# Kernel tuning notes

Hardware: AMD Instinct MI355X
Metric: run time of the kernel (lower is better)

The kernel has to match this reference:

```python
import jax, jax.numpy as jnp
import numpy as np

N_SAMPLES = 2048
BURN_IN = 128
STEP_SIZE = 0.1
D = 512   # walker dimension
H = 1024  # wavefunction MLP hidden width


def setup_inputs() -> dict:
    key = jax.random.key(0)
    k0, k1, k2 = jax.random.split(key, 3)
    x0 = jax.random.normal(k0, (1, D), dtype=jnp.float32)
    W1 = jax.random.normal(k1, (D, H), dtype=jnp.float32) / np.float32(np.sqrt(D))
    b1 = jnp.zeros((H,), dtype=jnp.float32)
    W2 = jax.random.normal(k2, (H, 1), dtype=jnp.float32) / np.float32(np.sqrt(H))
    b2 = jnp.zeros((1,), dtype=jnp.float32)
    return {"x0": x0, "W1": W1, "b1": b1, "W2": W2, "b2": b2}


def _model(x, W1, b1, W2, b2):
    # wavefunction MLP: [1, D] -> [1, 1]
    return jnp.tanh(x @ W1 + b1) @ W2 + b2


def reference(x0, W1, b1, W2, b2):
    def psi2(x):
        # model(x).pow(2)[0] -> shape [1]
        return (_model(x, W1, b1, W2, b2) ** 2)[0]

    def mh_step(x, k):
        k_noise, k_unif = jax.random.split(k)
        x_new = x + jax.random.normal(k_noise, x.shape, dtype=x.dtype) * STEP_SIZE
        p_new = psi2(x_new)
        p_old = psi2(x)
        ratio = jnp.minimum(p_new / (p_old + 1e-12), 1.0)          # clamp(max=1.0)
        u = jax.random.uniform(k_unif, ratio.shape, dtype=x.dtype)
        accept = (u < ratio).astype(x.dtype)[:, None]               # [1, 1]
        x = accept * x_new + (1.0 - accept) * x
        return x, x[0]  # carry chain state, record sample row [D]

    keys = jax.random.split(jax.random.key(1), N_SAMPLES + BURN_IN)
    _, traj = jax.lax.scan(mh_step, x0, keys)   # traj: [N+BURN_IN, D]
    return traj[BURN_IN:]                        # [N_SAMPLES, D]
```

## Files before the change

kernel.cpp:

```cpp
#include <hip/hip_runtime.h>
#include <stdint.h>
#include <math.h>


#define T_TOTAL 2176
#define NITER   1088
#define NROWS   2177
#define NBURN   128
#define DDIM    512
#define HDIM    1024
#define DONE_FLAG 0x13572468u

__device__ __forceinline__ uint2 tf2x32(uint32_t k0, uint32_t k1,
                                        uint32_t x0, uint32_t x1) {
  uint32_t ks2 = k0 ^ k1 ^ 0x1BD11BDAu;
  x0 += k0; x1 += k1;
#define TF_R(r) { x0 += x1; x1 = (x1 << (r)) | (x1 >> (32 - (r))); x1 ^= x0; }
  TF_R(13) TF_R(15) TF_R(26) TF_R(6)
  x0 += k1;  x1 += ks2 + 1u;
  TF_R(17) TF_R(29) TF_R(16) TF_R(24)
  x0 += ks2; x1 += k0 + 2u;
  TF_R(13) TF_R(15) TF_R(26) TF_R(6)
  x0 += k0;  x1 += k1 + 3u;
  TF_R(17) TF_R(29) TF_R(16) TF_R(24)
  x0 += k1;  x1 += ks2 + 4u;
  TF_R(13) TF_R(15) TF_R(26) TF_R(6)
  x0 += ks2; x1 += k0 + 5u;
#undef TF_R
  return make_uint2(x0, x1);
}

__device__ __forceinline__ float erfinv_xla(float x) {
  float w = -log1pf(-x * x);
  float p;
  if (w < 5.0f) {
    w = w - 2.5f;
    p = 2.81022636e-08f;
    p = fmaf(p, w, 3.43273939e-07f);
    p = fmaf(p, w, -3.5233877e-06f);
    p = fmaf(p, w, -4.39150654e-06f);
    p = fmaf(p, w, 0.00021858087f);
    p = fmaf(p, w, -0.00125372503f);
    p = fmaf(p, w, -0.00417768164f);
    p = fmaf(p, w, 0.246640727f);
    p = fmaf(p, w, 1.50140941f);
  } else {
    w = sqrtf(w) - 3.0f;
    p = -0.000200214257f;
    p = fmaf(p, w, 0.000100950558f);
    p = fmaf(p, w, 0.00134934322f);
    p = fmaf(p, w, -0.00367342844f);
    p = fmaf(p, w, 0.00573950773f);
    p = fmaf(p, w, -0.0076224613f);
    p = fmaf(p, w, 0.00943887047f);
    p = fmaf(p, w, 1.00167406f);
    p = fmaf(p, w, 2.83297682f);
  }
  return p * x;
}

__device__ __forceinline__ float normal_from_bits(uint32_t bits) {
  const float lo = -0.99999994f;
  float u01 = __uint_as_float(0x3f800000u | (bits >> 9)) - 1.0f;
  float v = u01 * 2.0f + lo;
  v = fmaxf(lo, v);
  return 1.41421356237309515f * erfinv_xla(v);
}

#if __has_builtin(__builtin_amdgcn_exp2f)
#define EXP2F __builtin_amdgcn_exp2f
#else
#define EXP2F exp2f
#endif
#define RCPF __builtin_amdgcn_rcpf
#define TANH_C 2.88539008177792681472f

__device__ __forceinline__ float tanh_fast(float x) {
  float a = x * TANH_C;
  float e = EXP2F(a);
  float r = RCPF(e + 1.0f);
  return fmaf(-2.0f, r, 1.0f);
}

__global__ void __launch_bounds__(256) rng_kernel(const float* __restrict__ x0,
                                                  float* __restrict__ A,
                                                  double* __restrict__ A64,
                                                  float* __restrict__ U) {
  const uint32_t t = blockIdx.x;
  const int tid = threadIdx.x;
  uint2 kt = tf2x32(0u, 1u, 0u, t);
  uint2 kn = tf2x32(kt.x, kt.y, 0u, 0u);
  uint2 e0 = tf2x32(kn.x, kn.y, 0u, (uint32_t)tid);
  uint2 e1 = tf2x32(kn.x, kn.y, 0u, (uint32_t)(tid + 256));
  float n0 = normal_from_bits(e0.x ^ e0.y) * 0.1f;
  float n1 = normal_from_bits(e1.x ^ e1.y) * 0.1f;
  float* Arow = A + (size_t)(t + 1) * DDIM;
  Arow[tid]       = n0;
  Arow[tid + 256] = n1;
  if (A64) {
    double* Arow64 = A64 + (size_t)(t + 1) * DDIM;
    Arow64[tid]       = (double)n0;
    Arow64[tid + 256] = (double)n1;
  }
  if (tid == 0) {
    uint2 ku = tf2x32(kt.x, kt.y, 0u, 1u);
    uint2 eu = tf2x32(ku.x, ku.y, 0u, 0u);
    U[t] = __uint_as_float(0x3f800000u | ((eu.x ^ eu.y) >> 9)) - 1.0f;
  }
  if (t == 0) {
    float xv0 = x0[tid], xv1 = x0[tid + 256];
    A[tid]       = xv0;
    A[tid + 256] = xv1;
    if (A64) {
      A64[tid]       = (double)xv0;
      A64[tid + 256] = (double)xv1;
    }
  }
}

__global__ void __launch_bounds__(512) gemm64_kernel(
    const double* __restrict__ A64, const float* __restrict__ W1,
    float* __restrict__ Z, int nrows) {
  const int r0 = blockIdx.x * 4;
  const int t  = threadIdx.x;
  const int c0 = t, c1 = t + 512;
  double acc[4][2];
#pragma unroll
  for (int r = 0; r < 4; ++r) { acc[r][0] = 0.0; acc[r][1] = 0.0; }
  for (int d = 0; d < 512; d += 4) {
    double wA[4], wB[4];
#pragma unroll
    for (int j = 0; j < 4; ++j) {
      wA[j] = (double)W1[(size_t)(d + j) * 1024 + c0];
      wB[j] = (double)W1[(size_t)(d + j) * 1024 + c1];
    }
#pragma unroll
    for (int r = 0; r < 4; ++r) {
      int rr = r0 + r; if (rr >= nrows) rr = nrows - 1;
      const double2 a01 = *(const double2*)(A64 + (size_t)rr * 512 + d);
      const double2 a23 = *(const double2*)(A64 + (size_t)rr * 512 + d + 2);
      acc[r][0] += (a01.x * wA[0] + a01.y * wA[1]) +
                   (a23.x * wA[2] + a23.y * wA[3]);
      acc[r][1] += (a01.x * wB[0] + a01.y * wB[1]) +
                   (a23.x * wB[2] + a23.y * wB[3]);
    }
  }
  const int rmax = (nrows - r0 < 4) ? (nrows - r0) : 4;
  for (int r = 0; r < rmax; ++r) {
    Z[(size_t)(r0 + r) * 1024 + c0] = (float)acc[r][0];
    Z[(size_t)(r0 + r) * 1024 + c1] = (float)acc[r][1];
  }
}

__global__ void __launch_bounds__(512) gemm_kernel(const float* __restrict__ A,
                                                   const float* __restrict__ W1,
                                                   float* __restrict__ Z,
                                                   int nrows) {
  const int r0 = blockIdx.x * 4;
  const int t  = threadIdx.x;
  const int c0 = t, c1 = t + 512;
  double acc[4][2];
#pragma unroll
  for (int r = 0; r < 4; ++r) { acc[r][0] = 0.0; acc[r][1] = 0.0; }
  for (int d = 0; d < 512; d += 4) {
    double wA[4], wB[4];
#pragma unroll
    for (int j = 0; j < 4; ++j) {
      wA[j] = (double)W1[(size_t)(d + j) * 1024 + c0];
      wB[j] = (double)W1[(size_t)(d + j) * 1024 + c1];
    }
#pragma unroll
    for (int r = 0; r < 4; ++r) {
      int rr = r0 + r; if (rr >= nrows) rr = nrows - 1;
      const float4 a4 = *(const float4*)(A + (size_t)rr * 512 + d);
      double a0 = (double)a4.x, a1 = (double)a4.y;
      double a2 = (double)a4.z, a3 = (double)a4.w;
      acc[r][0] += (a0 * wA[0] + a1 * wA[1]) + (a2 * wA[2] + a3 * wA[3]);
      acc[r][1] += (a0 * wB[0] + a1 * wB[1]) + (a2 * wB[2] + a3 * wB[3]);
    }
  }
  const int rmax = (nrows - r0 < 4) ? (nrows - r0) : 4;
  for (int r = 0; r < rmax; ++r) {
    Z[(size_t)(r0 + r) * 1024 + c0] = (float)acc[r][0];
    Z[(size_t)(r0 + r) * 1024 + c1] = (float)acc[r][1];
  }
}

#define DPP_STEP(v, ctrl)                                                    \
  v += __int_as_float(__builtin_amdgcn_update_dpp(                           \
      0, __float_as_int(v), (ctrl), 0xF, 0xF, true))

__device__ __forceinline__ float wave_reduce_to_last(float v) {
  DPP_STEP(v, 0xB1);
  DPP_STEP(v, 0x4E);
  DPP_STEP(v, 0x141);
  DPP_STEP(v, 0x140);
  DPP_STEP(v, 0x142);
  DPP_STEP(v, 0x143);
  return v;
}

__device__ __forceinline__ void wave_reduce3(float& a, float& b, float& c) {
#define R3(ctrl) { DPP_STEP(a, ctrl); DPP_STEP(b, ctrl); DPP_STEP(c, ctrl); }
  R3(0xB1) R3(0x4E) R3(0x141) R3(0x140) R3(0x142) R3(0x143)
#undef R3
}

__device__ __forceinline__ float psidot(double q0, double q1, double q2,
                                        double q3, float4 w2v) {
  float g0 = tanh_fast((float)q0), g1 = tanh_fast((float)q1);
  float g2 = tanh_fast((float)q2), g3 = tanh_fast((float)q3);
  return fmaf(g3, w2v.w, fmaf(g2, w2v.z, fmaf(g1, w2v.y, g0 * w2v.x)));
}

#define BAR() asm volatile("s_waitcnt lgkmcnt(0)\n\ts_barrier" ::: "memory")

#define EVAL3(NXT)                                                           \
  {                                                                          \
    float xA0 = (float)Ya0, xB0 = (float)Yb0, xC0 = (float)Yc0;              \
    float xA1 = (float)Ya1, xB1 = (float)Yb1, xC1 = (float)Yc1;              \
    float xA2 = (float)Ya2, xB2 = (float)Yb2, xC2 = (float)Yc2;              \
    float xA3 = (float)Ya3, xB3 = (float)Yb3, xC3 = (float)Yc3;              \
    float aA0 = xA0 * TANH_C, aB0 = xB0 * TANH_C, aC0 = xC0 * TANH_C;        \
    float aA1 = xA1 * TANH_C, aB1 = xB1 * TANH_C, aC1 = xC1 * TANH_C;        \
    float aA2 = xA2 * TANH_C, aB2 = xB2 * TANH_C, aC2 = xC2 * TANH_C;        \
    float aA3 = xA3 * TANH_C, aB3 = xB3 * TANH_C, aC3 = xC3 * TANH_C;        \
    float eA0 = EXP2F(aA0), eB0 = EXP2F(aB0), eC0 = EXP2F(aC0);              \
    float eA1 = EXP2F(aA1), eB1 = EXP2F(aB1), eC1 = EXP2F(aC1);              \
    float eA2 = EXP2F(aA2), eB2 = EXP2F(aB2), eC2 = EXP2F(aC2);              \
    float eA3 = EXP2F(aA3), eB3 = EXP2F(aB3), eC3 = EXP2F(aC3);              \
    float sA0 = eA0 + 1.0f, sB0 = eB0 + 1.0f, sC0 = eC0 + 1.0f;              \
    float sA1 = eA1 + 1.0f, sB1 = eB1 + 1.0f, sC1 = eC1 + 1.0f;              \
    float sA2 = eA2 + 1.0f, sB2 = eB2 + 1.0f, sC2 = eC2 + 1.0f;              \
    float sA3 = eA3 + 1.0f, sB3 = eB3 + 1.0f, sC3 = eC3 + 1.0f;              \
    float rA0 = RCPF(sA0), rB0 = RCPF(sB0), rC0 = RCPF(sC0);                 \
    float rA1 = RCPF(sA1), rB1 = RCPF(sB1), rC1 = RCPF(sC1);                 \
    float rA2 = RCPF(sA2), rB2 = RCPF(sB2), rC2 = RCPF(sC2);                 \
    float rA3 = RCPF(sA3), rB3 = RCPF(sB3), rC3 = RCPF(sC3);                 \
    float gA0 = fmaf(-2.0f, rA0, 1.0f), gB0 = fmaf(-2.0f, rB0, 1.0f);        \
    float gC0 = fmaf(-2.0f, rC0, 1.0f);                                      \
    float gA1 = fmaf(-2.0f, rA1, 1.0f), gB1 = fmaf(-2.0f, rB1, 1.0f);        \
    float gC1 = fmaf(-2.0f, rC1, 1.0f);                                      \
    float gA2 = fmaf(-2.0f, rA2, 1.0f), gB2 = fmaf(-2.0f, rB2, 1.0f);        \
    float gC2 = fmaf(-2.0f, rC2, 1.0f);                                      \
    float gA3 = fmaf(-2.0f, rA3, 1.0f), gB3 = fmaf(-2.0f, rB3, 1.0f);        \
    float gC3 = fmaf(-2.0f, rC3, 1.0f);                                      \
    float tA = gA0 * w2v.x, tB = gB0 * w2v.x, tC = gC0 * w2v.x;              \
    tA = fmaf(gA1, w2v.y, tA); tB = fmaf(gB1, w2v.y, tB);                    \
    tC = fmaf(gC1, w2v.y, tC);                                               \
    tA = fmaf(gA2, w2v.z, tA); tB = fmaf(gB2, w2v.z, tB);                    \
    tC = fmaf(gC2, w2v.z, tC);                                               \
    tA = fmaf(gA3, w2v.w, tA); tB = fmaf(gB3, w2v.w, tB);                    \
    tC = fmaf(gC3, w2v.w, tC);                                               \
    wave_reduce3(tA, tB, tC);                                                \
    if (lane == 63) {                                                        \
      wsum[NXT][0][wid] = tA;                                                \
      wsum[NXT][1][wid] = tB;                                                \
      wsum[NXT][2][wid] = tC;                                                \
    }                                                                        \
  }

__global__ void __launch_bounds__(256, 1) chain_kernel(
    const float* __restrict__ Z, const float* __restrict__ A,
    const float* __restrict__ U, const float* __restrict__ x0,
    const float* __restrict__ b1, const float* __restrict__ W2,
    const float* __restrict__ b2, float* __restrict__ out,
    unsigned* __restrict__ flag) {
  const int tid = threadIdx.x;

  if (blockIdx.x != 0) {
    float acc = (float)tid * 1.0e-6f;
    for (int i = 0; i < 4000; ++i) {
#pragma unroll
      for (int jj = 0; jj < 256; ++jj) acc = fmaf(acc, 0.99999988f, 1.0e-7f);
      unsigned f = __hip_atomic_load(flag, __ATOMIC_RELAXED,
                                     __HIP_MEMORY_SCOPE_AGENT);
      if (f == DONE_FLAG) break;
    }
    if (acc == 123456.75f && tid == 1023) out[0] = acc;
    return;
  }

  const int lane = tid & 63;
  const int wid = tid >> 6;
  __shared__ __align__(16) float wsum[2][3][4];
  __shared__ float Uld[2184];

  const float4* Zv = (const float4*)Z;
  const float2* Av = (const float2*)A;

  for (int i = tid; i < 2184; i += 256) Uld[i] = U[i];

  const float4 w2v = ((const float4*)W2)[tid];
  const float4 b1v = ((const float4*)b1)[tid];
  const float b2v = b2[0];

  float4 z0r = Zv[tid];
  float4 z1r = Zv[256 + tid];
  float4 z2r = Zv[512 + tid];
  float4 zA0 = Zv[3 * 256 + tid], zB0 = Zv[4 * 256 + tid];
  float4 zA1 = Zv[5 * 256 + tid], zB1 = Zv[6 * 256 + tid];
  float2 dAa0 = Av[1 * 256 + tid], dAb0 = Av[2 * 256 + tid];
  float2 dAa1 = Av[3 * 256 + tid], dAb1 = Av[4 * 256 + tid];

  double Y0 = (double)z0r.x + (double)b1v.x;
  double Y1 = (double)z0r.y + (double)b1v.y;
  double Y2 = (double)z0r.z + (double)b1v.z;
  double Y3 = (double)z0r.w + (double)b1v.w;

  float xa = x0[2 * tid], xb = x0[2 * tid + 1];

  __syncthreads();

  {
    float tm = psidot(Y0, Y1, Y2, Y3, w2v);
    tm = wave_reduce_to_last(tm);
    if (lane == 63) wsum[1][0][wid] = tm;
  }
  __syncthreads();
  float p;
  {
    const float4 pp = *(const float4*)wsum[1][0];
    float m0 = ((pp.x + pp.y) + (pp.z + pp.w)) + b2v;
    p = m0 * m0;
  }
  float um1 = Uld[0] * (p + 1e-12f);
  float u2c = Uld[1];

  double Ya0 = Y0 + (double)z1r.x, Ya1 = Y1 + (double)z1r.y;
  double Ya2 = Y2 + (double)z1r.z, Ya3 = Y3 + (double)z1r.w;
  double Yb0 = Y0 + (double)z2r.x, Yb1 = Y1 + (double)z2r.y;
  double Yb2 = Y2 + (double)z2r.z, Yb3 = Y3 + (double)z2r.w;
  double Yc0 = Ya0 + (double)z2r.x, Yc1 = Ya1 + (double)z2r.y;
  double Yc2 = Ya2 + (double)z2r.z, Yc3 = Ya3 + (double)z2r.w;
  EVAL3(0)
  __syncthreads();

#define ITER(k, PAR, ZAB, ZBB, DAB, DBB)                                     \
  {                                                                          \
    float u1n = Uld[2 * (k) + 2];                                            \
    float u2n = Uld[2 * (k) + 3];                                            \
    const float4 e1 = *(const float4*)wsum[PAR][0];                          \
    const float4 e2 = *(const float4*)wsum[PAR][1];                          \
    const float4 e3 = *(const float4*)wsum[PAR][2];                          \
    float m1 = ((e1.x + e1.y) + (e1.z + e1.w)) + b2v;                        \
    float q1 = m1 * m1;                                                      \
    bool a1v = um1 < q1;                                                     \
    float p1 = a1v ? q1 : p;                                                 \
    float um2 = u2c * (p1 + 1e-12f);                                         \
    float m2v = ((e2.x + e2.y) + (e2.z + e2.w)) + b2v;                       \
    float m3v = ((e3.x + e3.y) + (e3.z + e3.w)) + b2v;                       \
    float m23 = a1v ? m3v : m2v;                                             \
    float q23 = m23 * m23;                                                   \
    bool a2v = um2 < q23;                                                    \
    p = a2v ? q23 : p1;                                                      \
    float xat = a1v ? xa + DAB.x : xa;                                       \
    float xbt = a1v ? xb + DAB.y : xb;                                       \
    xa = a2v ? xat + DBB.x : xat;                                            \
    xb = a2v ? xbt + DBB.y : xbt;                                            \
    if ((k) >= 64) {                                                         \
      float2 o1; o1.x = xat; o1.y = xbt;                                     \
      *(float2*)(out + (size_t)(2 * (k) - NBURN) * DDIM + 2 * tid) = o1;     \
      float2 o2; o2.x = xa; o2.y = xb;                                       \
      *(float2*)(out + (size_t)(2 * (k) + 1 - NBURN) * DDIM + 2 * tid) = o2; \
    }                                                                        \
    DAB = Av[(size_t)(2 * (k) + 5) * 256 + tid];                             \
    DBB = Av[(size_t)(2 * (k) + 6) * 256 + tid];                             \
    Y0 = a1v ? (a2v ? Yc0 : Ya0) : (a2v ? Yb0 : Y0);                         \
    Y1 = a1v ? (a2v ? Yc1 : Ya1) : (a2v ? Yb1 : Y1);                         \
    Y2 = a1v ? (a2v ? Yc2 : Ya2) : (a2v ? Yb2 : Y2);                         \
    Y3 = a1v ? (a2v ? Yc3 : Ya3) : (a2v ? Yb3 : Y3);                         \
    Ya0 = Y0 + (double)ZAB.x;  Ya1 = Y1 + (double)ZAB.y;                     \
    Ya2 = Y2 + (double)ZAB.z;  Ya3 = Y3 + (double)ZAB.w;                     \
    Yb0 = Y0 + (double)ZBB.x;  Yb1 = Y1 + (double)ZBB.y;                     \
    Yb2 = Y2 + (double)ZBB.z;  Yb3 = Y3 + (double)ZBB.w;                     \
    Yc0 = Ya0 + (double)ZBB.x; Yc1 = Ya1 + (double)ZBB.y;                    \
    Yc2 = Ya2 + (double)ZBB.z; Yc3 = Ya3 + (double)ZBB.w;                    \
    ZAB = Zv[(size_t)(2 * (k) + 7) * 256 + tid];                             \
    ZBB = Zv[(size_t)(2 * (k) + 8) * 256 + tid];                             \
    EVAL3((PAR) ^ 1)                                                         \
    um1 = u1n * (p + 1e-12f);                                                \
    u2c = u2n;                                                               \
    BAR();                                                                   \
  }

  for (int k = 0; k < NITER; k += 2) {
    ITER(k,     0, zA0, zB0, dAa0, dAb0);
    ITER(k + 1, 1, zA1, zB1, dAa1, dAb1);
  }
#undef ITER

  if (tid == 0) {
    __hip_atomic_store(flag, DONE_FLAG, __ATOMIC_RELAXED,
                       __HIP_MEMORY_SCOPE_AGENT);
  }
}

extern "C" void kernel_launch(void* const* d_in, const int* in_sizes, int n_in,
                              void* d_out, int out_size, void* d_ws, size_t ws_size,
                              hipStream_t stream) {
  const float* x0 = (const float*)d_in[0];
  const float* W1 = (const float*)d_in[1];
  const float* b1 = (const float*)d_in[2];
  const float* W2 = (const float*)d_in[3];
  const float* b2 = (const float*)d_in[4];
  float* out = (float*)d_out;

  char* ws = (char*)d_ws;
  float* A = (float*)ws;
  float* Z = (float*)(ws + 4472832);
  float* U = (float*)(ws + 4472832 + 8945664);
  unsigned* flag = (unsigned*)(ws + 4472832 + 8945664 + 8736);
  size_t a64_off = 13427328;
  double* A64 = (double*)(ws + a64_off);
  bool use64 = (ws_size >= a64_off + (size_t)2184 * 512 * 8);

  rng_kernel<<<T_TOTAL, 256, 0, stream>>>(x0, A, use64 ? A64 : (double*)nullptr, U);
  if (use64)
    gemm64_kernel<<<546, 512, 0, stream>>>(A64, W1, Z, NROWS);
  else
    gemm_kernel<<<546, 512, 0, stream>>>(A, W1, Z, NROWS);
  chain_kernel<<<256, 256, 0, stream>>>(Z, A, U, x0, b1, W2, b2, out, flag);
}
```

Before: 803.3 us.

## Fuse fp64 projection GEMM into chain kernel with per-group ready flags

Removes the separate gemm64 launch. The 255 idle helper blocks of the chain kernel now compute the fp64 x@W1 rows in groups of four and publish a per-group release flag. The sequential chain block spin-waits on these flags just before it loads each Z row, so the GEMM overlaps with the serial MH chain instead of running before it. This adds acquire/release polling and relies on all blocks being co-resident. The helper GEMM uses 256 threads per group instead of 512, so it may lag the chain early on.

```diff
diff --git a/kernel.cpp b/kernel.cpp
--- a/kernel.cpp
+++ b/kernel.cpp
@@ -9,6 +9,7 @@
 #define NBURN   128
 #define DDIM    512
 #define HDIM    1024
+#define NGRP    546
 #define DONE_FLAG 0x13572468u
 
 __device__ __forceinline__ uint2 tf2x32(uint32_t k0, uint32_t k1,
@@ -85,7 +86,8 @@
 __global__ void __launch_bounds__(256) rng_kernel(const float* __restrict__ x0,
                                                   float* __restrict__ A,
                                                   double* __restrict__ A64,
-                                                  float* __restrict__ U) {
+                                                  float* __restrict__ U,
+                                                  unsigned* __restrict__ zflag) {
   const uint32_t t = blockIdx.x;
   const int tid = threadIdx.x;
   uint2 kt = tf2x32(0u, 1u, 0u, t);
@@ -115,7 +117,44 @@
       A64[tid]       = (double)xv0;
       A64[tid + 256] = (double)xv1;
     }
-  }
+    if (zflag) {
+      for (int i = tid; i < NGRP; i += 256) zflag[i] = 0u;
+    }
+  }
+}
+
+__device__ __forceinline__ void gemm64_rows4(
+    const double* __restrict__ A64, const float* __restrict__ W1,
+    float* __restrict__ Z, int g, int tid) {
+  const int r0 = g * 4;
+  double acc[4][4];
+#pragma unroll
+  for (int r = 0; r < 4; ++r)
+#pragma unroll
+    for (int q = 0; q < 4; ++q) acc[r][q] = 0.0;
+  for (int d = 0; d < 512; d += 4) {
+    double w[4][4];
+#pragma unroll
+    for (int j = 0; j < 4; ++j)
+#pragma unroll
+      for (int q = 0; q < 4; ++q)
+        w[j][q] = (double)W1[(size_t)(d + j) * 1024 + (tid + q * 256)];
+#pragma unroll
+    for (int r = 0; r < 4; ++r) {
+      int rr = r0 + r; if (rr >= NROWS) rr = NROWS - 1;
+      const double2 a01 = *(const double2*)(A64 + (size_t)rr * 512 + d);
+      const double2 a23 = *(const double2*)(A64 + (size_t)rr * 512 + d + 2);
+#pragma unroll
+      for (int q = 0; q < 4; ++q)
+        acc[r][q] += (a01.x * w[0][q] + a01.y * w[1][q]) +
+                     (a23.x * w[2][q] + a23.y * w[3][q]);
+    }
+  }
+  const int rmax = (NROWS - r0 < 4) ? (NROWS - r0) : 4;
+  for (int r = 0; r < rmax; ++r)
+#pragma unroll
+    for (int q = 0; q < 4; ++q)
+      Z[(size_t)(r0 + r) * 1024 + (tid + q * 256)] = (float)acc[r][q];
 }
 
 __global__ void __launch_bounds__(512) gemm64_kernel(
@@ -260,15 +299,36 @@
     }                                                                        \
   }
 
+#define ZWAIT(g)                                                             \
+  if ((g) > wm) {                                                            \
+    while (wm < (g)) {                                                       \
+      if (__hip_atomic_load(&zflag[wm + 1], __ATOMIC_ACQUIRE,                \
+                            __HIP_MEMORY_SCOPE_AGENT) != 0u) ++wm;           \
+      else __builtin_amdgcn_s_sleep(2);                                      \
+    }                                                                        \
+  }
+
 __global__ void __launch_bounds__(256, 1) chain_kernel(
     const float* __restrict__ Z, const float* __restrict__ A,
     const float* __restrict__ U, const float* __restrict__ x0,
     const float* __restrict__ b1, const float* __restrict__ W2,
     const float* __restrict__ b2, float* __restrict__ out,
-    unsigned* __restrict__ flag) {
+    unsigned* __restrict__ flag, const double* __restrict__ A64,
+    const float* __restrict__ W1, float* __restrict__ Zw,
+    unsigned* __restrict__ zflag) {
   const int tid = threadIdx.x;
 
   if (blockIdx.x != 0) {
+    if (zflag) {
+      for (int g = (int)blockIdx.x - 1; g < NGRP; g += 255) {
+        gemm64_rows4(A64, W1, Zw, g, tid);
+        __threadfence();
+        __syncthreads();
+        if (tid == 0)
+          __hip_atomic_store(&zflag[g], 1u, __ATOMIC_RELEASE,
+                             __HIP_MEMORY_SCOPE_AGENT);
+      }
+    }
     float acc = (float)tid * 1.0e-6f;
     for (int i = 0; i < 4000; ++i) {
 #pragma unroll
@@ -295,6 +355,9 @@
   const float4 b1v = ((const float4*)b1)[tid];
   const float b2v = b2[0];
 
+  int wm = zflag ? -1 : (1 << 30);
+
+  ZWAIT(1)
   float4 z0r = Zv[tid];
   float4 z1r = Zv[256 + tid];
   float4 z2r = Zv[512 + tid];
@@ -376,6 +439,7 @@
     Yb2 = Y2 + (double)ZBB.z;  Yb3 = Y3 + (double)ZBB.w;                     \
     Yc0 = Ya0 + (double)ZBB.x; Yc1 = Ya1 + (double)ZBB.y;                    \
     Yc2 = Ya2 + (double)ZBB.z; Yc3 = Ya3 + (double)ZBB.w;                    \
+    ZWAIT(((2 * (k) + 8) >> 2))                                              \
     ZAB = Zv[(size_t)(2 * (k) + 7) * 256 + tid];                             \
     ZBB = Zv[(size_t)(2 * (k) + 8) * 256 + tid];                             \
     EVAL3((PAR) ^ 1)                                                         \
@@ -413,12 +477,26 @@
   unsigned* flag = (unsigned*)(ws + 4472832 + 8945664 + 8736);
   size_t a64_off = 13427328;
   double* A64 = (double*)(ws + a64_off);
-  bool use64 = (ws_size >= a64_off + (size_t)2184 * 512 * 8);
-
-  rng_kernel<<<T_TOTAL, 256, 0, stream>>>(x0, A, use64 ? A64 : (double*)nullptr, U);
-  if (use64)
+  size_t zf_off = a64_off + (size_t)2184 * 512 * 8;
+  unsigned* zflag = (unsigned*)(ws + zf_off);
+  bool use64 = (ws_size >= zf_off);
+  bool inl   = (ws_size >= zf_off + NGRP * sizeof(unsigned));
+
+  rng_kernel<<<T_TOTAL, 256, 0, stream>>>(
+      x0, A, use64 ? A64 : (double*)nullptr, U,
+      (use64 && inl) ? zflag : (unsigned*)nullptr);
+
+  if (use64 && inl) {
+    chain_kernel<<<256, 256, 0, stream>>>(Z, A, U, x0, b1, W2, b2, out, flag,
+                                          A64, W1, Z, zflag);
+  } else if (use64) {
     gemm64_kernel<<<546, 512, 0, stream>>>(A64, W1, Z, NROWS);
-  else
+    chain_kernel<<<256, 256, 0, stream>>>(Z, A, U, x0, b1, W2, b2, out, flag,
+                                          A64, W1, Z, (unsigned*)nullptr);
+  } else {
     gemm_kernel<<<546, 512, 0, stream>>>(A, W1, Z, NROWS);
-  chain_kernel<<<256, 256, 0, stream>>>(Z, A, U, x0, b1, W2, b2, out, flag);
-}
+    chain_kernel<<<256, 256, 0, stream>>>(Z, A, U, x0, b1, W2, b2, out, flag,
+                                          (const double*)A, W1, Z,
+                                          (unsigned*)nullptr);
+  }
+}
```

New measurement: 1.035 ms. 28.8% more time.

## Fuse RNG generation into GEMM kernel with shared-memory double rows

Applied to the files above, without the earlier changes.

Merges the noise-generation kernel into the fp64 GEMM. Each block now generates its own 4 rows of normals (plus uniforms) directly into an LDS double buffer instead of writing and rereading a global double-precision A64 buffer. This removes one kernel launch and the global round-trip of the fp64 activations. In exchange the RNG work is serialized at the start of each GEMM block, and each thread computes one normal per row instead of two per thread.

```diff
diff --git a/kernel.cpp b/kernel.cpp
--- a/kernel.cpp
+++ b/kernel.cpp
@@ -82,47 +82,42 @@
   return fmaf(-2.0f, r, 1.0f);
 }
 
-__global__ void __launch_bounds__(256) rng_kernel(const float* __restrict__ x0,
-                                                  float* __restrict__ A,
-                                                  double* __restrict__ A64,
-                                                  float* __restrict__ U) {
-  const uint32_t t = blockIdx.x;
-  const int tid = threadIdx.x;
-  uint2 kt = tf2x32(0u, 1u, 0u, t);
-  uint2 kn = tf2x32(kt.x, kt.y, 0u, 0u);
-  uint2 e0 = tf2x32(kn.x, kn.y, 0u, (uint32_t)tid);
-  uint2 e1 = tf2x32(kn.x, kn.y, 0u, (uint32_t)(tid + 256));
-  float n0 = normal_from_bits(e0.x ^ e0.y) * 0.1f;
-  float n1 = normal_from_bits(e1.x ^ e1.y) * 0.1f;
-  float* Arow = A + (size_t)(t + 1) * DDIM;
-  Arow[tid]       = n0;
-  Arow[tid + 256] = n1;
-  if (A64) {
-    double* Arow64 = A64 + (size_t)(t + 1) * DDIM;
-    Arow64[tid]       = (double)n0;
-    Arow64[tid + 256] = (double)n1;
-  }
-  if (tid == 0) {
-    uint2 ku = tf2x32(kt.x, kt.y, 0u, 1u);
-    uint2 eu = tf2x32(ku.x, ku.y, 0u, 0u);
-    U[t] = __uint_as_float(0x3f800000u | ((eu.x ^ eu.y) >> 9)) - 1.0f;
-  }
-  if (t == 0) {
-    float xv0 = x0[tid], xv1 = x0[tid + 256];
-    A[tid]       = xv0;
-    A[tid + 256] = xv1;
-    if (A64) {
-      A64[tid]       = (double)xv0;
-      A64[tid + 256] = (double)xv1;
-    }
-  }
-}
-
-__global__ void __launch_bounds__(512) gemm64_kernel(
-    const double* __restrict__ A64, const float* __restrict__ W1,
-    float* __restrict__ Z, int nrows) {
-  const int r0 = blockIdx.x * 4;
-  const int t  = threadIdx.x;
+__global__ void __launch_bounds__(512) rnggemm_kernel(
+    const float* __restrict__ x0, const float* __restrict__ W1,
+    float* __restrict__ A, float* __restrict__ U, float* __restrict__ Z) {
+  const int g = blockIdx.x;
+  const int t = threadIdx.x;
+  __shared__ __align__(16) double As64[4][512];
+
+#pragma unroll
+  for (int i = 0; i < 4; ++i) {
+    const int r  = 4 * g + i;
+    const int rr = (r < NROWS) ? r : (NROWS - 1);
+    float val;
+    if (rr == 0) {
+      val = x0[t];
+    } else {
+      const uint32_t tt = (uint32_t)(rr - 1);
+      uint2 kt = tf2x32(0u, 1u, 0u, tt);
+      uint2 kn = tf2x32(kt.x, kt.y, 0u, 0u);
+      uint2 e0 = tf2x32(kn.x, kn.y, 0u, (uint32_t)t);
+      val = normal_from_bits(e0.x ^ e0.y) * 0.1f;
+    }
+    As64[i][t] = (double)val;
+    if (r < NROWS) A[(size_t)r * DDIM + t] = val;
+  }
+  if (t < 4) {
+    const int tu = 4 * g + t;
+    if (tu < T_TOTAL) {
+      uint2 kt = tf2x32(0u, 1u, 0u, (uint32_t)tu);
+      uint2 ku = tf2x32(kt.x, kt.y, 0u, 1u);
+      uint2 eu = tf2x32(ku.x, ku.y, 0u, 0u);
+      U[tu] = __uint_as_float(0x3f800000u | ((eu.x ^ eu.y) >> 9)) - 1.0f;
+    }
+  }
+  __syncthreads();
+
+  const int r0 = g * 4;
   const int c0 = t, c1 = t + 512;
   double acc[4][2];
 #pragma unroll
@@ -136,50 +131,15 @@
     }
 #pragma unroll
     for (int r = 0; r < 4; ++r) {
-      int rr = r0 + r; if (rr >= nrows) rr = nrows - 1;
-      const double2 a01 = *(const double2*)(A64 + (size_t)rr * 512 + d);
-      const double2 a23 = *(const double2*)(A64 + (size_t)rr * 512 + d + 2);
+      const double2 a01 = *(const double2*)&As64[r][d];
+      const double2 a23 = *(const double2*)&As64[r][d + 2];
       acc[r][0] += (a01.x * wA[0] + a01.y * wA[1]) +
                    (a23.x * wA[2] + a23.y * wA[3]);
       acc[r][1] += (a01.x * wB[0] + a01.y * wB[1]) +
                    (a23.x * wB[2] + a23.y * wB[3]);
     }
   }
-  const int rmax = (nrows - r0 < 4) ? (nrows - r0) : 4;
-  for (int r = 0; r < rmax; ++r) {
-    Z[(size_t)(r0 + r) * 1024 + c0] = (float)acc[r][0];
-    Z[(size_t)(r0 + r) * 1024 + c1] = (float)acc[r][1];
-  }
-}
-
-__global__ void __launch_bounds__(512) gemm_kernel(const float* __restrict__ A,
-                                                   const float* __restrict__ W1,
-                                                   float* __restrict__ Z,
-                                                   int nrows) {
-  const int r0 = blockIdx.x * 4;
-  const int t  = threadIdx.x;
-  const int c0 = t, c1 = t + 512;
-  double acc[4][2];
-#pragma unroll
-  for (int r = 0; r < 4; ++r) { acc[r][0] = 0.0; acc[r][1] = 0.0; }
-  for (int d = 0; d < 512; d += 4) {
-    double wA[4], wB[4];
-#pragma unroll
-    for (int j = 0; j < 4; ++j) {
-      wA[j] = (double)W1[(size_t)(d + j) * 1024 + c0];
-      wB[j] = (double)W1[(size_t)(d + j) * 1024 + c1];
-    }
-#pragma unroll
-    for (int r = 0; r < 4; ++r) {
-      int rr = r0 + r; if (rr >= nrows) rr = nrows - 1;
-      const float4 a4 = *(const float4*)(A + (size_t)rr * 512 + d);
-      double a0 = (double)a4.x, a1 = (double)a4.y;
-      double a2 = (double)a4.z, a3 = (double)a4.w;
-      acc[r][0] += (a0 * wA[0] + a1 * wA[1]) + (a2 * wA[2] + a3 * wA[3]);
-      acc[r][1] += (a0 * wB[0] + a1 * wB[1]) + (a2 * wB[2] + a3 * wB[3]);
-    }
-  }
-  const int rmax = (nrows - r0 < 4) ? (nrows - r0) : 4;
+  const int rmax = (NROWS - r0 < 4) ? (NROWS - r0) : 4;
   for (int r = 0; r < rmax; ++r) {
     Z[(size_t)(r0 + r) * 1024 + c0] = (float)acc[r][0];
     Z[(size_t)(r0 + r) * 1024 + c1] = (float)acc[r][1];
@@ -411,14 +371,7 @@
   float* Z = (float*)(ws + 4472832);
   float* U = (float*)(ws + 4472832 + 8945664);
   unsigned* flag = (unsigned*)(ws + 4472832 + 8945664 + 8736);
-  size_t a64_off = 13427328;
-  double* A64 = (double*)(ws + a64_off);
-  bool use64 = (ws_size >= a64_off + (size_t)2184 * 512 * 8);
-
-  rng_kernel<<<T_TOTAL, 256, 0, stream>>>(x0, A, use64 ? A64 : (double*)nullptr, U);
-  if (use64)
-    gemm64_kernel<<<546, 512, 0, stream>>>(A64, W1, Z, NROWS);
-  else
-    gemm_kernel<<<546, 512, 0, stream>>>(A, W1, Z, NROWS);
+
+  rnggemm_kernel<<<545, 512, 0, stream>>>(x0, W1, A, U, Z);
   chain_kernel<<<256, 256, 0, stream>>>(Z, A, U, x0, b1, W2, b2, out, flag);
 }
```

Result: no change. 809.4 us (+0.8%).
